# Kernel tuning notes

Measured on AMD Instinct MI355X. Metric: run time of the kernel, lower is better.

Reference implementation:

```python
import jax, jax.numpy as jnp
import numpy as np

B = 32768  # batch of sudoku puzzles

def _pair_matrices():
    # 36 = C(9,2) digit-pair permutations, exactly as in the torch __init__
    enc = np.zeros((36, 9), dtype=np.float32)
    dec = np.zeros((9, 36), dtype=np.float32)
    count = 0
    for i in range(8):
        for j in range(i + 1, 9):
            enc[count, i] = 1.0
            enc[count, j] = 1.0
            dec[i, count] = 1.0
            dec[j, count] = 1.0
            count += 1
    return enc, dec

def nn_and(x, y):
    return jnp.clip(jnp.minimum(x, y), 0.0, 1.0)

def nn_compare(x, value):
    # triangular bump: 1 at x==value, 0 outside (value-1, value+1)
    a = jax.nn.relu(x - value + 1.0)
    b = jax.nn.relu(value + 1.0 - x)
    return jnp.minimum(a, b)

def setup_inputs() -> dict:
    key = jax.random.key(0)
    # binary candidate mask: mask[b, d, r, c] == 1 iff digit d is still possible at (r, c)
    mask = jnp.round(jax.random.uniform(key, (B, 9, 9, 9), dtype=jnp.float32))
    enc, dec = _pair_matrices()
    return {"mask": mask, "enc_w": jnp.asarray(enc), "dec_w": jnp.asarray(dec)}

def reference(mask, enc_w, dec_w):
    # encode_permutations: 1x1 conv 9 -> 36 channels
    perm = jnp.einsum("oc,bchw->bohw", enc_w, mask)          # [B,36,9,9]
    perm = nn_compare(perm, 2.0)                              # cell has exactly this digit-pair
    # sum_all_permutations: 1x1 conv 36 -> 1 with all-ones weight
    s = jnp.sum(perm, axis=1, keepdims=True)                  # [B,1,9,9]
    s = nn_compare(s, 1.0)
    perm = nn_and(perm, s)                                    # broadcast over 36 channels
    # type 'h': grouped (1,9) all-ones conv = sum over width
    down = jnp.sum(perm, axis=3, keepdims=True)               # [B,36,9,1]
    down = nn_compare(down, 2.0)
    # UpsamplingNearest2d(scale_factor=(1,9)) of a width-1 map = broadcast
    up = jnp.broadcast_to(down, perm.shape)                   # [B,36,9,9]
    up = nn_and(up, 1.0 - perm)                               # NNNot(perm)
    # decode_permutations: 1x1 conv 36 -> 9
    erase = jnp.einsum("oc,bchw->bohw", dec_w, up)            # [B,9,9,9]
    return nn_and(mask, 1.0 - erase)
```

## Files before the change

### kernel.cpp

```cpp
#include <hip/hip_runtime.h>
#include <stdint.h>


#define GBATCH 8
#define WORDS_PER_WG (GBATCH * 729)
#define CHUNKS (WORDS_PER_WG / 4)

typedef uint32_t u32x4 __attribute__((ext_vector_type(4)));
typedef const __attribute__((address_space(1))) uint32_t* gsrc_t;
typedef __attribute__((address_space(3))) uint32_t* lptr_t;

__global__ __launch_bounds__(256) void sudoku_kernel(
    const uint32_t* __restrict__ in, uint32_t* __restrict__ out) {
  __shared__ uint32_t lds[WORDS_PER_WG];
  const int g = blockIdx.x;
  const int t = threadIdx.x;
  const uint32_t* gin = in + (size_t)g * WORDS_PER_WG;

#pragma unroll
  for (int j = 0; j < 6; ++j) {
    int i = t + j * 256;
    if (i < CHUNKS) {
      __builtin_amdgcn_global_load_lds((gsrc_t)(gin + i * 4),
                                       (lptr_t)(&lds[i * 4]), 16, 0, 0);
    }
  }
  __syncthreads();

  if (t < GBATCH * 9) {
    const int bl = t / 9;
    const int h = t - bl * 9;
    const int rbase = bl * 729 + h * 9;

    uint32_t cand[9];
#pragma unroll
    for (int w = 0; w < 9; ++w) cand[w] = 0u;
#pragma unroll
    for (int d = 0; d < 9; ++d) {
#pragma unroll
      for (int w = 0; w < 9; ++w)
        cand[w] |= (lds[rbase + d * 81 + w] ? 1u : 0u) << d;
    }

    uint32_t clearbits[9];
#pragma unroll
    for (int w = 0; w < 9; ++w) clearbits[w] = 0u;
#pragma unroll
    for (int w1 = 0; w1 < 9; ++w1) {
      uint32_t c1 = cand[w1];
      if (__popc(c1) != 2) continue;
      int cnt = 0;
#pragma unroll
      for (int w2 = 0; w2 < 9; ++w2) cnt += (cand[w2] == c1) ? 1 : 0;
      if (cnt == 2) {
#pragma unroll
        for (int w = 0; w < 9; ++w)
          if (cand[w] != c1) clearbits[w] |= c1;
      }
    }

    uint32_t keep[9];
#pragma unroll
    for (int w = 0; w < 9; ++w) keep[w] = cand[w] & ~clearbits[w];

#pragma unroll
    for (int d = 0; d < 9; ++d) {
#pragma unroll
      for (int w = 0; w < 9; ++w)
        lds[rbase + d * 81 + w] =
            ((keep[w] >> d) & 1u) ? 0x3F800000u : 0u;
    }
  }
  __syncthreads();

  uint32_t* gout = out + (size_t)g * WORDS_PER_WG;
#pragma unroll
  for (int j = 0; j < 6; ++j) {
    int i = t + j * 256;
    if (i < CHUNKS) {
      u32x4 v = {lds[i * 4], lds[i * 4 + 1], lds[i * 4 + 2], lds[i * 4 + 3]};
      *(u32x4*)(gout + i * 4) = v;
    }
  }
}

extern "C" void kernel_launch(void* const* d_in, const int* in_sizes, int n_in,
                              void* d_out, int out_size, void* d_ws, size_t ws_size,
                              hipStream_t stream) {
  const uint32_t* in = (const uint32_t*)d_in[0];
  uint32_t* out = (uint32_t*)d_out;
  int B = in_sizes[0] / 729;
  int blocks = B / GBATCH;
  sudoku_kernel<<<blocks, 256, 0, stream>>>(in, out);
}
```

Before: 35.03 us.

## Make each wave process its own puzzles independently, removing block barriers

Restructures the kernel so each 64-lane wave owns four puzzles in a private LDS slice. It loads them asynchronously, waits only on its own vmcnt, computes, and writes back with no workgroup barriers. The LDS readback is also changed to one 16-byte vector read instead of four scalar reads. This aims to remove __syncthreads stalls and let waves overlap load, compute and store. Risks are that lane-wise LDS ordering relies on intra-wave execution without an explicit LDS wait, and that only 36 of 64 lanes are active in compute.

```diff
diff --git a/kernel.cpp b/kernel.cpp
--- a/kernel.cpp
+++ b/kernel.cpp
@@ -2,34 +2,39 @@
 #include <stdint.h>
 
 
-#define GBATCH 8
-#define WORDS_PER_WG (GBATCH * 729)
-#define CHUNKS (WORDS_PER_WG / 4)
+#define WAVE_BATCHES 4
+#define WAVE_WORDS (WAVE_BATCHES * 729)
+#define WAVE_CHUNKS (WAVE_WORDS / 4)
+#define WAVES_PER_WG 4
 
 typedef uint32_t u32x4 __attribute__((ext_vector_type(4)));
 typedef const __attribute__((address_space(1))) uint32_t* gsrc_t;
 typedef __attribute__((address_space(3))) uint32_t* lptr_t;
 
 __global__ __launch_bounds__(256) void sudoku_kernel(
-    const uint32_t* __restrict__ in, uint32_t* __restrict__ out) {
-  __shared__ uint32_t lds[WORDS_PER_WG];
-  const int g = blockIdx.x;
-  const int t = threadIdx.x;
-  const uint32_t* gin = in + (size_t)g * WORDS_PER_WG;
+    const uint32_t* __restrict__ in, uint32_t* __restrict__ out, int nwaves) {
+  __shared__ __align__(16) uint32_t lds[WAVES_PER_WG][WAVE_WORDS];
+  const int lane = threadIdx.x & 63;
+  const int wslot = threadIdx.x >> 6;
+  const int wave_id = blockIdx.x * WAVES_PER_WG + wslot;
+  if (wave_id >= nwaves) return;
+
+  const uint32_t* gin = in + (size_t)wave_id * WAVE_WORDS;
+  uint32_t* lbase = &lds[wslot][0];
 
 #pragma unroll
-  for (int j = 0; j < 6; ++j) {
-    int i = t + j * 256;
-    if (i < CHUNKS) {
+  for (int j = 0; j < 12; ++j) {
+    int i = lane + j * 64;
+    if (i < WAVE_CHUNKS) {
       __builtin_amdgcn_global_load_lds((gsrc_t)(gin + i * 4),
-                                       (lptr_t)(&lds[i * 4]), 16, 0, 0);
+                                       (lptr_t)(lbase + i * 4), 16, 0, 0);
     }
   }
-  __syncthreads();
+  asm volatile("s_waitcnt vmcnt(0)" ::: "memory");
 
-  if (t < GBATCH * 9) {
-    const int bl = t / 9;
-    const int h = t - bl * 9;
+  if (lane < WAVE_BATCHES * 9) {
+    const int bl = lane / 9;
+    const int h = lane - bl * 9;
     const int rbase = bl * 729 + h * 9;
 
     uint32_t cand[9];
@@ -39,7 +44,7 @@
     for (int d = 0; d < 9; ++d) {
 #pragma unroll
       for (int w = 0; w < 9; ++w)
-        cand[w] |= (lds[rbase + d * 81 + w] ? 1u : 0u) << d;
+        cand[w] |= (lbase[rbase + d * 81 + w] ? 1u : 0u) << d;
     }
 
     uint32_t clearbits[9];
@@ -67,18 +72,16 @@
     for (int d = 0; d < 9; ++d) {
 #pragma unroll
       for (int w = 0; w < 9; ++w)
-        lds[rbase + d * 81 + w] =
-            ((keep[w] >> d) & 1u) ? 0x3F800000u : 0u;
+        lbase[rbase + d * 81 + w] = ((keep[w] >> d) & 1u) ? 0x3F800000u : 0u;
     }
   }
-  __syncthreads();
 
-  uint32_t* gout = out + (size_t)g * WORDS_PER_WG;
+  uint32_t* gout = out + (size_t)wave_id * WAVE_WORDS;
 #pragma unroll
-  for (int j = 0; j < 6; ++j) {
-    int i = t + j * 256;
-    if (i < CHUNKS) {
-      u32x4 v = {lds[i * 4], lds[i * 4 + 1], lds[i * 4 + 2], lds[i * 4 + 3]};
+  for (int j = 0; j < 12; ++j) {
+    int i = lane + j * 64;
+    if (i < WAVE_CHUNKS) {
+      u32x4 v = *(const u32x4*)(lbase + i * 4);
       *(u32x4*)(gout + i * 4) = v;
     }
   }
@@ -90,6 +93,7 @@
   const uint32_t* in = (const uint32_t*)d_in[0];
   uint32_t* out = (uint32_t*)d_out;
   int B = in_sizes[0] / 729;
-  int blocks = B / GBATCH;
-  sudoku_kernel<<<blocks, 256, 0, stream>>>(in, out);
+  int nwaves = (B + WAVE_BATCHES - 1) / WAVE_BATCHES;
+  int blocks = (nwaves + WAVES_PER_WG - 1) / WAVES_PER_WG;
+  sudoku_kernel<<<blocks, 256, 0, stream>>>(in, out, nwaves);
 }
```

Result: no change. 35.56 us (+1.5%).
